# Performance work log

Hardware: AMD Instinct MI355X
Metric: run time of the kernel (lower is better)

The kernel has to match this reference:

```python
import jax, jax.numpy as jnp
import numpy as np

B, S, D, H = 4, 2048, 1024, 16
HD = D // H  # head_dim = 64


def rope(x):
    # canonical interleaved RoPE over the full feature dim, applied pre-head-split
    # x: [B, S, D]
    d = x.shape[-1]
    inv_freq = 1.0 / (10000.0 ** (jnp.arange(0, d, 2, dtype=jnp.float32) / d))  # [D/2]
    pos = jnp.arange(x.shape[1], dtype=jnp.float32)
    ang = pos[:, None] * inv_freq[None, :]          # [S, D/2]
    cos, sin = jnp.cos(ang), jnp.sin(ang)
    x1, x2 = x[..., 0::2], x[..., 1::2]             # even/odd pairs
    r1 = x1 * cos - x2 * sin
    r2 = x1 * sin + x2 * cos
    return jnp.stack([r1, r2], axis=-1).reshape(x.shape)


def setup_inputs() -> dict:
    key = jax.random.key(0)
    ks = jax.random.split(key, 9)
    s = 1.0 / np.sqrt(D)
    def lin(k):
        kw, kb = jax.random.split(k)
        W = jax.random.uniform(kw, (D, D), jnp.float32, -s, s)
        b = jax.random.uniform(kb, (D,), jnp.float32, -s, s)
        return W, b
    Wq, bq = lin(ks[0]); Wk, bk = lin(ks[1]); Wv, bv = lin(ks[2]); W0, b0 = lin(ks[3])
    x = jax.random.normal(ks[4], (B, S, D), jnp.float32)
    return {"x": x, "Wq": Wq, "bq": bq, "Wk": Wk, "bk": bk,
            "Wv": Wv, "bv": bv, "W0": W0, "b0": b0}


def reference(x, Wq, bq, Wk, bk, Wv, bv, W0, b0):
    # QKV projections (torch Linear: x @ W.T + b; here W stored as [in, out])
    q = x @ Wq + bq
    k = x @ Wk + bk
    v = x @ Wv + bv
    # RoPE applied to full d_model before head split (as in the source)
    q = rope(q)
    k = rope(k)
    # split heads -> [B, H, S, HD]
    b, s, _ = x.shape
    qh = q.reshape(b, s, H, HD).transpose(0, 2, 1, 3)
    kh = k.reshape(b, s, H, HD).transpose(0, 2, 1, 3)
    vh = v.reshape(b, s, H, HD).transpose(0, 2, 1, 3)
    scores = jnp.einsum("bhqd,bhkd->bhqk", qh, kh) / jnp.sqrt(jnp.float32(HD))
    attn = jax.nn.softmax(scores, axis=-1)  # dropout p=0.0 -> identity
    out = jnp.einsum("bhqk,bhkd->bhqd", attn, vh)
    out = out.transpose(0, 2, 1, 3).reshape(b, s, D)
    return out @ W0 + b0
```

## Files before the change

kernel.cpp:

```cpp
#include <hip/hip_runtime.h>
#include <hip/hip_bf16.h>

typedef unsigned short u16;
typedef u16 u16x8 __attribute__((ext_vector_type(8)));
typedef float f32x4 __attribute__((ext_vector_type(4)));
typedef __bf16 bf16x8 __attribute__((ext_vector_type(8)));

#define B_ 4
#define S_ 2048
#define D_ 1024
#define H_ 16
#define HD_ 64
#define M_ (B_*S_)

#if __has_builtin(__builtin_amdgcn_exp2f)
#define EXP2(x) __builtin_amdgcn_exp2f(x)
#else
#define EXP2(x) exp2f(x)
#endif

__device__ __forceinline__ f32x4 MFMA(u16x8 a, u16x8 b, f32x4 c) {
  return __builtin_amdgcn_mfma_f32_16x16x32_bf16(
      __builtin_bit_cast(bf16x8, a), __builtin_bit_cast(bf16x8, b), c, 0, 0, 0);
}

__device__ __forceinline__ u16 f2b(float f) {
  return __builtin_bit_cast(u16, __float2bfloat16(f));
}

__device__ __forceinline__ void load_lds16(const void* g, void* l) {
  __builtin_amdgcn_global_load_lds(
      (const __attribute__((address_space(1))) void*)g,
      (__attribute__((address_space(3))) void*)l, 16, 0, 0);
}

__device__ __forceinline__ unsigned int cvtpk(float lo, float hi) {
  unsigned int r;
  asm("v_cvt_pk_bf16_f32 %0, %1, %2" : "=v"(r) : "v"(lo), "v"(hi));
  return r;
}

__global__ __launch_bounds__(256) void k_rope_tab(float2* __restrict__ tab) {
  int i = blockIdx.x * 256 + threadIdx.x;
  if (i >= S_ * (D_ / 2)) return;
  int s = i >> 9;
  int f = i & 511;
  float invf = exp2f((float)f * (-13.287712379549449f / 512.0f));
  float ang = (float)s * invf;
  tab[i] = make_float2(cosf(ang), sinf(ang));
}

__global__ __launch_bounds__(256) void k_cvt(const float* __restrict__ x,
                                             u16* __restrict__ xb, int n) {
  int i = blockIdx.x * 256 + threadIdx.x;
  if (i * 4 >= n) return;
  float4 v = ((const float4*)x)[i];
  ushort4 o;
  o.x = f2b(v.x); o.y = f2b(v.y); o.z = f2b(v.z); o.w = f2b(v.w);
  ((ushort4*)xb)[i] = o;
}

__global__ __launch_bounds__(256) void k_transpose4(
    const float* __restrict__ Wq, const float* __restrict__ Wk,
    const float* __restrict__ Wv, const float* __restrict__ W0,
    u16* __restrict__ Tq, u16* __restrict__ Tk, u16* __restrict__ Tv,
    u16* __restrict__ T0) {
  const float* W = (blockIdx.z == 0) ? Wq : (blockIdx.z == 1) ? Wk
                   : (blockIdx.z == 2) ? Wv : W0;
  u16* WT = (blockIdx.z == 0) ? Tq : (blockIdx.z == 1) ? Tk
            : (blockIdx.z == 2) ? Tv : T0;
  __shared__ float t[32][33];
  int tx = threadIdx.x, ty = threadIdx.y;
  int bx = blockIdx.x * 32, by = blockIdx.y * 32;
#pragma unroll
  for (int j = 0; j < 32; j += 8)
    t[ty + j][tx] = W[(size_t)(by + ty + j) * D_ + bx + tx];
  __syncthreads();
#pragma unroll
  for (int j = 0; j < 32; j += 8)
    WT[(size_t)(bx + ty + j) * D_ + by + tx] = f2b(t[tx][ty + j]);
}

__global__ __launch_bounds__(512, 2) void k_gemm256_qkv(
    const u16* __restrict__ A, const u16* __restrict__ BT,
    const float* __restrict__ bq, const float* __restrict__ bk,
    const float* __restrict__ bv, const float2* __restrict__ tab,
    u16* __restrict__ Qh, u16* __restrict__ Kh, u16* __restrict__ Vt) {
  __shared__ __attribute__((aligned(16))) u16 Al0[16384], Al1[16384];
  __shared__ __attribute__((aligned(16))) u16 Bl0[16384], Bl1[16384];
  const int tid = threadIdx.x;
  const int lane = tid & 63, wid = tid >> 6;
  const int wm = wid >> 2, wn = wid & 3;
  const int g = lane >> 4, c = lane & 15;
  const int flat = blockIdx.x;
  const int xcd = flat & 7, idx = flat >> 3;
  const int bx = xcd * 4 + (idx & 3), by = idx >> 2;
  const int rowbase = bx * 256;

  const int rr_ = tid >> 3, slot = tid & 7;
  const int sw8 = slot ^ (rr_ & 7);
  const u16* aB = A + (size_t)(rowbase + rr_) * 1024 + sw8 * 8;
  const u16* bB = BT + (size_t)(by * 256 + rr_) * 1024 + sw8 * 8;
  const int wdst = wid * 512;

  f32x4 acc[8][4] = {};
  const int swz = (c & 7) << 3;
  const int k0o = (g * 8) ^ swz;
  const int k1o = k0o ^ 32;
  const int ArdB = (wm * 128 + c) * 64;
  const int BrdB = (wn * 64 + c) * 64;

  u16x8 bf00, bf01, bf10, bf11, bf20, bf21, bf30, bf31;

#define ISSUE_LO(NA, NB, KT)                                                 \
  load_lds16(aB + (KT), &NA[wdst]);                                          \
  load_lds16(aB + 65536 + (KT), &NA[4096 + wdst]);                           \
  load_lds16(bB + (KT), &NB[wdst]);                                          \
  load_lds16(bB + 65536 + (KT), &NB[4096 + wdst]);
#define ISSUE_HI(NA, NB, KT)                                                 \
  load_lds16(aB + 131072 + (KT), &NA[8192 + wdst]);                          \
  load_lds16(aB + 196608 + (KT), &NA[12288 + wdst]);                         \
  load_lds16(bB + 131072 + (KT), &NB[8192 + wdst]);                          \
  load_lds16(bB + 196608 + (KT), &NB[12288 + wdst]);
#define PBAR                                                                 \
  __builtin_amdgcn_sched_barrier(0);                                         \
  __builtin_amdgcn_s_barrier();                                              \
  asm volatile("s_waitcnt lgkmcnt(0)" ::: "memory");                         \
  __builtin_amdgcn_sched_barrier(0);                                         \
  __builtin_amdgcn_s_setprio(1);
#define PEND                                                                 \
  __builtin_amdgcn_s_setprio(0);                                             \
  __builtin_amdgcn_sched_barrier(0);                                         \
  __builtin_amdgcn_s_barrier();
#define LDB8(CB)                                                             \
  bf00 = *(const u16x8*)&CB[BrdB + k0o];                                     \
  bf01 = *(const u16x8*)&CB[BrdB + k1o];                                     \
  bf10 = *(const u16x8*)&CB[BrdB + 1024 + k0o];                              \
  bf11 = *(const u16x8*)&CB[BrdB + 1024 + k1o];                              \
  bf20 = *(const u16x8*)&CB[BrdB + 2048 + k0o];                              \
  bf21 = *(const u16x8*)&CB[BrdB + 2048 + k1o];                              \
  bf30 = *(const u16x8*)&CB[BrdB + 3072 + k0o];                              \
  bf31 = *(const u16x8*)&CB[BrdB + 3072 + k1o];
#define LDA4(CA, MI0)                                                        \
  a00 = *(const u16x8*)&CA[ArdB + (MI0) * 1024 + k0o];                       \
  a01 = *(const u16x8*)&CA[ArdB + (MI0) * 1024 + k1o];                       \
  a10 = *(const u16x8*)&CA[ArdB + (MI0 + 1) * 1024 + k0o];                   \
  a11 = *(const u16x8*)&CA[ArdB + (MI0 + 1) * 1024 + k1o];
#define MFMA16(MI0)                                                          \
  acc[MI0][0] = MFMA(a00, bf00, acc[MI0][0]);                                \
  acc[MI0][0] = MFMA(a01, bf01, acc[MI0][0]);                                \
  acc[MI0][1] = MFMA(a00, bf10, acc[MI0][1]);                                \
  acc[MI0][1] = MFMA(a01, bf11, acc[MI0][1]);                                \
  acc[MI0][2] = MFMA(a00, bf20, acc[MI0][2]);                                \
  acc[MI0][2] = MFMA(a01, bf21, acc[MI0][2]);                                \
  acc[MI0][3] = MFMA(a00, bf30, acc[MI0][3]);                                \
  acc[MI0][3] = MFMA(a01, bf31, acc[MI0][3]);                                \
  acc[MI0 + 1][0] = MFMA(a10, bf00, acc[MI0 + 1][0]);                        \
  acc[MI0 + 1][0] = MFMA(a11, bf01, acc[MI0 + 1][0]);                        \
  acc[MI0 + 1][1] = MFMA(a10, bf10, acc[MI0 + 1][1]);                        \
  acc[MI0 + 1][1] = MFMA(a11, bf11, acc[MI0 + 1][1]);                        \
  acc[MI0 + 1][2] = MFMA(a10, bf20, acc[MI0 + 1][2]);                        \
  acc[MI0 + 1][2] = MFMA(a11, bf21, acc[MI0 + 1][2]);                        \
  acc[MI0 + 1][3] = MFMA(a10, bf30, acc[MI0 + 1][3]);                        \
  acc[MI0 + 1][3] = MFMA(a11, bf31, acc[MI0 + 1][3]);
#define TILE(CA, CB, NA, NB, KT, STG)                                        \
  {                                                                          \
    u16x8 a00, a01, a10, a11;                                                \
    if (STG) { ISSUE_LO(NA, NB, KT) }                                        \
    LDB8(CB) LDA4(CA, 0)                                                     \
    PBAR MFMA16(0) PEND                                                      \
    if (STG) { ISSUE_HI(NA, NB, KT) }                                        \
    LDA4(CA, 2) PBAR MFMA16(2) PEND                                          \
    LDA4(CA, 4) PBAR MFMA16(4) PEND                                          \
    LDA4(CA, 6) PBAR MFMA16(6)                                               \
    __builtin_amdgcn_s_setprio(0);                                           \
    __syncthreads();                                                         \
  }

  ISSUE_LO(Al0, Bl0, 0)
  ISSUE_HI(Al0, Bl0, 0)
  __syncthreads();

#pragma unroll 1
  for (int it = 0; it < 7; ++it) {
    const int kt1 = (2 * it + 1) * 64, kt2 = (2 * it + 2) * 64;
    TILE(Al0, Bl0, Al1, Bl1, kt1, 1)
    TILE(Al1, Bl1, Al0, Bl0, kt2, 1)
  }
  TILE(Al0, Bl0, Al1, Bl1, 15 * 64, 1)
  TILE(Al1, Bl1, Al0, Bl0, 0, 0)

  const int mode = by >> 2;
  const float* bias = (mode == 0) ? bq : (mode == 1) ? bk : bv;
  u16* Cout = (mode == 0) ? Qh : (mode == 1) ? Kh : Vt;
  const int colL0 = (by & 3) * 256 + wn * 64;
  int coln[4];
  float bn[4];
#pragma unroll
  for (int ni = 0; ni < 4; ++ni) {
    coln[ni] = colL0 + ni * 16 + c;
    bn[ni] = bias[coln[ni]];
  }
  if (mode == 2) {
#pragma unroll
    for (int mi = 0; mi < 8; ++mi) {
      const int row0 = rowbase + wm * 128 + mi * 16 + g * 4;
      const int s0 = row0 & (S_ - 1);
      const int bidx = row0 >> 11;
#pragma unroll
      for (int ni = 0; ni < 4; ++ni) {
        const int h = coln[ni] >> 6, hd = coln[ni] & 63;
        ushort4 w;
        w.x = f2b(acc[mi][ni][0] + bn[ni]);
        w.y = f2b(acc[mi][ni][1] + bn[ni]);
        w.z = f2b(acc[mi][ni][2] + bn[ni]);
        w.w = f2b(acc[mi][ni][3] + bn[ni]);
        *(ushort4*)(Cout + ((size_t)(bidx * H_ + h) * HD_ + hd) * S_ + s0) = w;
      }
    }
  } else {
    const float qs = 0.18033688011112042f;
#pragma unroll
    for (int mi = 0; mi < 8; ++mi) {
#pragma unroll
      for (int rq = 0; rq < 4; ++rq) {
        const int row = rowbase + wm * 128 + mi * 16 + g * 4 + rq;
        const int s = row & (S_ - 1);
        const int bidx = row >> 11;
#pragma unroll
        for (int ni = 0; ni < 4; ++ni) {
          float v = acc[mi][ni][rq] + bn[ni];
          float2 cs = tab[(size_t)s * 512 + (coln[ni] >> 1)];
          float nb = __shfl_xor(v, 1);
          v = (lane & 1) ? (nb * cs.y + v * cs.x) : (v * cs.x - nb * cs.y);
          if (mode == 0) v *= qs;
          const int h = coln[ni] >> 6, hd = coln[ni] & 63;
          Cout[(((size_t)(bidx * H_ + h)) * S_ + s) * HD_ + hd] = f2b(v);
        }
      }
    }
  }
#undef TILE
#undef MFMA16
#undef LDA4
#undef LDB8
#undef PEND
#undef PBAR
#undef ISSUE_HI
#undef ISSUE_LO
}

__global__ __launch_bounds__(256, 2) void k_gemm_o(
    const u16* __restrict__ A, const u16* __restrict__ BT,
    const float* __restrict__ bias, float* __restrict__ Cout) {
  __shared__ __attribute__((aligned(16))) u16 Al[128 * 64];
  __shared__ __attribute__((aligned(16))) u16 Bl[128 * 64];
  const int tid = threadIdx.x;
  const int lane = tid & 63, wid = tid >> 6;
  const int wr = wid >> 1, wc = wid & 1;
  const int g = lane >> 4, c = lane & 15;
  const int flat = blockIdx.y * gridDim.x + blockIdx.x;
  const int xcd = flat & 7, idx = flat >> 3;
  const int bx = xcd * 8 + (idx & 7), by = idx >> 3;
  const int rowbase = bx * 128, colbase = by * 128;

  f32x4 acc[4][4] = {};
  const int ldr = lane >> 3;
  const int ldk = (lane & 7) * 8;

  for (int kt = 0; kt < D_; kt += 64) {
    __syncthreads();
#pragma unroll
    for (int j = 0; j < 4; ++j) {
      const int chunk = wid * 4 + j;
      const int rr = chunk * 8 + ldr;
      load_lds16(A + (size_t)(rowbase + rr) * D_ + kt + ldk, &Al[chunk * 512]);
      load_lds16(BT + (size_t)(colbase + rr) * D_ + kt + ldk, &Bl[chunk * 512]);
    }
    __syncthreads();
#pragma unroll
    for (int ks = 0; ks < 2; ++ks) {
      u16x8 a[4], b[4];
#pragma unroll
      for (int m = 0; m < 4; ++m)
        a[m] = *(const u16x8*)&Al[(wr * 64 + m * 16 + c) * 64 + ks * 32 + g * 8];
#pragma unroll
      for (int n = 0; n < 4; ++n)
        b[n] = *(const u16x8*)&Bl[(wc * 64 + n * 16 + c) * 64 + ks * 32 + g * 8];
#pragma unroll
      for (int m = 0; m < 4; ++m)
#pragma unroll
        for (int n = 0; n < 4; ++n)
          acc[m][n] = MFMA(a[m], b[n], acc[m][n]);
    }
  }

  int coln[4];
  float bn[4];
#pragma unroll
  for (int n = 0; n < 4; ++n) {
    coln[n] = colbase + wc * 64 + n * 16 + c;
    bn[n] = bias[coln[n]];
  }
#pragma unroll
  for (int m = 0; m < 4; ++m)
#pragma unroll
    for (int r = 0; r < 4; ++r) {
      const int row = rowbase + wr * 64 + m * 16 + g * 4 + r;
#pragma unroll
      for (int n = 0; n < 4; ++n)
        Cout[(size_t)row * D_ + coln[n]] = acc[m][n][r] + bn[n];
    }
}

__global__ __launch_bounds__(512, 4) void k_attn(const u16* __restrict__ Qh,
                                                 const u16* __restrict__ Kh,
                                                 const u16* __restrict__ Vt,
                                                 u16* __restrict__ AO) {
  __shared__ __attribute__((aligned(16))) u16 Kl0[4096], Kl1[4096];
  __shared__ __attribute__((aligned(16))) u16 Vl0[4096], Vl1[4096];
  __shared__ __attribute__((aligned(16))) u16 Pl[16384];
  const int tid = threadIdx.x;
  const int lane = tid & 63, wid = tid >> 6;
  const int g = lane >> 4, c = lane & 15;
  const int flat = blockIdx.x;
  const int swzid = (flat & 7) * 64 + (flat >> 3);
  const int bh = swzid >> 3, qt = swzid & 7;
  const size_t base = (size_t)bh * S_ * HD_;
  const int qr0 = qt * 256 + wid * 32;

  u16x8 qf[2][2];
#pragma unroll
  for (int qg = 0; qg < 2; ++qg)
#pragma unroll
    for (int ks = 0; ks < 2; ++ks)
      qf[qg][ks] = *(const u16x8*)(Qh + base +
                                   (size_t)(qr0 + qg * 16 + c) * HD_ +
                                   ks * 32 + g * 8);

  f32x4 o20[4] = {}, o21[4] = {};
  float L0 = 0.f, L1 = 0.f;

  const int swz = (c & 7) << 3;
  const int kb0 = c * 64 + ((g * 8) ^ swz);
  const int kb1 = c * 64 + ((32 + g * 8) ^ swz);
  const int pwA0 = wid * 2048 + ((c * 64 + 0 * 16 + g * 4) ^ swz);
  const int pwA1 = wid * 2048 + ((c * 64 + 1 * 16 + g * 4) ^ swz);
  const int pwA2 = wid * 2048 + ((c * 64 + 2 * 16 + g * 4) ^ swz);
  const int pwA3 = wid * 2048 + ((c * 64 + 3 * 16 + g * 4) ^ swz);
  const int pbA0 = wid * 2048 + kb0;
  const int pbA1 = wid * 2048 + kb1;
  const f32x4 z4 = {0.f, 0.f, 0.f, 0.f};

  const int ldrow = lane >> 3, ldslot = lane & 7;
  const int srow = wid * 8 + ldrow;
  const u16* kp0 = Kh + base + (size_t)srow * HD_ + (ldslot ^ (srow & 7)) * 8;
  const u16* vp0 = Vt + base + (size_t)srow * S_ + (ldslot ^ (srow & 7)) * 8;
  const int kdst0 = wid * 512;

#define STAGE(KP, VP)                                                        \
  {                                                                          \
    load_lds16(kp0, &KP[kdst0]); kp0 += 64 * HD_;                            \
    load_lds16(vp0, &VP[kdst0]); vp0 += 64;                                  \
  }

#define BODY(KC, VC, KP, VP)                                                 \
  {                                                                          \
    STAGE(KP, VP);                                                           \
    f32x4 s40[4], s41[4];                                                    \
    __builtin_amdgcn_s_setprio(1);                                           \
    _Pragma("unroll") for (int n = 0; n < 4; ++n) {                          \
      u16x8 kfa = *(const u16x8*)&KC[n * 1024 + kb0];                        \
      u16x8 kfb = *(const u16x8*)&KC[n * 1024 + kb1];                        \
      s40[n] = MFMA(kfa, qf[0][0], z4);                                      \
      s40[n] = MFMA(kfb, qf[0][1], s40[n]);                                  \
      s41[n] = MFMA(kfa, qf[1][0], z4);                                      \
      s41[n] = MFMA(kfb, qf[1][1], s41[n]);                                  \
    }                                                                        \
    __builtin_amdgcn_s_setprio(0);                                           \
    float rs0 = 0.f, rs1 = 0.f;                                              \
    _Pragma("unroll") for (int n = 0; n < 4; ++n) {                          \
      float p0[4], p1[4];                                                    \
      _Pragma("unroll") for (int r = 0; r < 4; ++r) {                        \
        p0[r] = EXP2(s40[n][r]); rs0 += p0[r];                               \
        p1[r] = EXP2(s41[n][r]); rs1 += p1[r];                               \
      }                                                                      \
      uint2 w0, w1;                                                          \
      w0.x = cvtpk(p0[0], p0[1]); w0.y = cvtpk(p0[2], p0[3]);                \
      w1.x = cvtpk(p1[0], p1[1]); w1.y = cvtpk(p1[2], p1[3]);                \
      const int pw = (n == 0) ? pwA0 : (n == 1) ? pwA1 : (n == 2) ? pwA2     \
                                                                  : pwA3;   \
      *(uint2*)&Pl[pw] = w0;                                                 \
      *(uint2*)&Pl[pw + 1024] = w1;                                          \
    }                                                                        \
    L0 += rs0; L1 += rs1;                                                    \
    asm volatile("s_waitcnt lgkmcnt(0)" ::: "memory");                       \
    __builtin_amdgcn_sched_barrier(0);                                       \
    __builtin_amdgcn_s_setprio(1);                                           \
    {                                                                        \
      u16x8 pa00 = *(const u16x8*)&Pl[pbA0];                                 \
      u16x8 pa01 = *(const u16x8*)&Pl[pbA1];                                 \
      u16x8 pa10 = *(const u16x8*)&Pl[pbA0 + 1024];                          \
      u16x8 pa11 = *(const u16x8*)&Pl[pbA1 + 1024];                          \
      _Pragma("unroll") for (int nd = 0; nd < 4; ++nd) {                     \
        u16x8 va0 = *(const u16x8*)&VC[nd * 1024 + kb0];                     \
        u16x8 va1 = *(const u16x8*)&VC[nd * 1024 + kb1];                     \
        o20[nd] = MFMA(va0, pa00, o20[nd]);                                  \
        o20[nd] = MFMA(va1, pa01, o20[nd]);                                  \
        o21[nd] = MFMA(va0, pa10, o21[nd]);                                  \
        o21[nd] = MFMA(va1, pa11, o21[nd]);                                  \
      }                                                                      \
    }                                                                        \
    __builtin_amdgcn_s_setprio(0);                                           \
    __syncthreads();                                                         \
  }

  STAGE(Kl0, Vl0);
  __syncthreads();

#pragma unroll 1
  for (int it = 0; it < 16; ++it) {
    BODY(Kl0, Vl0, Kl1, Vl1);
    BODY(Kl1, Vl1, Kl0, Vl0);
  }

  L0 += __shfl_xor(L0, 16);
  L0 += __shfl_xor(L0, 32);
  L1 += __shfl_xor(L1, 16);
  L1 += __shfl_xor(L1, 32);
  const float inv0 = 1.f / L0, inv1 = 1.f / L1;
  const int b = bh >> 4, h = bh & (H_ - 1);
#pragma unroll
  for (int nd = 0; nd < 4; ++nd) {
    ushort4 w;
    w.x = f2b(o20[nd][0] * inv0);
    w.y = f2b(o20[nd][1] * inv0);
    w.z = f2b(o20[nd][2] * inv0);
    w.w = f2b(o20[nd][3] * inv0);
    *(ushort4*)(AO + ((size_t)(b * S_ + qr0 + c)) * D_ + h * HD_ + nd * 16 +
                g * 4) = w;
    ushort4 w2;
    w2.x = f2b(o21[nd][0] * inv1);
    w2.y = f2b(o21[nd][1] * inv1);
    w2.z = f2b(o21[nd][2] * inv1);
    w2.w = f2b(o21[nd][3] * inv1);
    *(ushort4*)(AO + ((size_t)(b * S_ + qr0 + 16 + c)) * D_ + h * HD_ +
                nd * 16 + g * 4) = w2;
  }
#undef BODY
#undef STAGE
}

extern "C" void kernel_launch(void* const* d_in, const int* in_sizes, int n_in,
                              void* d_out, int out_size, void* d_ws,
                              size_t ws_size, hipStream_t stream) {
  const float* x  = (const float*)d_in[0];
  const float* Wq = (const float*)d_in[1];
  const float* bq = (const float*)d_in[2];
  const float* Wk = (const float*)d_in[3];
  const float* bk = (const float*)d_in[4];
  const float* Wv = (const float*)d_in[5];
  const float* bv = (const float*)d_in[6];
  const float* W0 = (const float*)d_in[7];
  const float* b0 = (const float*)d_in[8];
  float* out = (float*)d_out;

  char* ws = (char*)d_ws;
  const size_t MiB = (size_t)1 << 20;
  float2* tab = (float2*)(ws + 0);
  u16* xb  = (u16*)(ws + 8 * MiB);
  u16* WqT = (u16*)(ws + 24 * MiB);
  u16* WkT = (u16*)(ws + 26 * MiB);
  u16* WvT = (u16*)(ws + 28 * MiB);
  u16* W0T = (u16*)(ws + 30 * MiB);
  u16* Qh  = (u16*)(ws + 32 * MiB);
  u16* Kh  = (u16*)(ws + 48 * MiB);
  u16* Vt  = (u16*)(ws + 64 * MiB);
  u16* AO  = (u16*)(ws + 80 * MiB);

  k_rope_tab<<<4096, 256, 0, stream>>>(tab);
  k_cvt<<<(M_ * D_ / 4 + 255) / 256, 256, 0, stream>>>(x, xb, M_ * D_);
  k_transpose4<<<dim3(32, 32, 4), dim3(32, 8), 0, stream>>>(
      Wq, Wk, Wv, W0, WqT, WkT, WvT, W0T);
  k_gemm256_qkv<<<384, 512, 0, stream>>>(xb, WqT, bq, bk, bv, tab, Qh, Kh, Vt);
  k_attn<<<512, 512, 0, stream>>>(Qh, Kh, Vt, AO);
  k_gemm_o<<<dim3(64, 8), 256, 0, stream>>>(AO, W0T, b0, out);
}
```

Baseline: 191.5 us.

## Merge prep kernels into one launch and single-buffer the QKV GEMM LDS

Combines the RoPE table, input bf16 conversion and weight transpose kernels into a single k_prep launch that dispatches on block index, saving two kernel launches. The QKV GEMM drops its LDS double buffer: each k-step now issues all global-to-LDS loads, waits at a barrier, then computes. This halves LDS use, which may allow more resident blocks, but it removes the overlap of the next tile's loads with the current MFMA work, so load latency is exposed on every k iteration.

```diff
diff --git a/kernel.cpp b/kernel.cpp
--- a/kernel.cpp
+++ b/kernel.cpp
@@ -40,45 +40,43 @@
   return r;
 }
 
-__global__ __launch_bounds__(256) void k_rope_tab(float2* __restrict__ tab) {
-  int i = blockIdx.x * 256 + threadIdx.x;
-  if (i >= S_ * (D_ / 2)) return;
-  int s = i >> 9;
-  int f = i & 511;
-  float invf = exp2f((float)f * (-13.287712379549449f / 512.0f));
-  float ang = (float)s * invf;
-  tab[i] = make_float2(cosf(ang), sinf(ang));
-}
-
-__global__ __launch_bounds__(256) void k_cvt(const float* __restrict__ x,
-                                             u16* __restrict__ xb, int n) {
-  int i = blockIdx.x * 256 + threadIdx.x;
-  if (i * 4 >= n) return;
-  float4 v = ((const float4*)x)[i];
-  ushort4 o;
-  o.x = f2b(v.x); o.y = f2b(v.y); o.z = f2b(v.z); o.w = f2b(v.w);
-  ((ushort4*)xb)[i] = o;
-}
-
-__global__ __launch_bounds__(256) void k_transpose4(
+__global__ __launch_bounds__(256) void k_prep(
+    const float* __restrict__ x, u16* __restrict__ xb,
     const float* __restrict__ Wq, const float* __restrict__ Wk,
     const float* __restrict__ Wv, const float* __restrict__ W0,
     u16* __restrict__ Tq, u16* __restrict__ Tk, u16* __restrict__ Tv,
-    u16* __restrict__ T0) {
-  const float* W = (blockIdx.z == 0) ? Wq : (blockIdx.z == 1) ? Wk
-                   : (blockIdx.z == 2) ? Wv : W0;
-  u16* WT = (blockIdx.z == 0) ? Tq : (blockIdx.z == 1) ? Tk
-            : (blockIdx.z == 2) ? Tv : T0;
+    u16* __restrict__ T0, float2* __restrict__ tab) {
   __shared__ float t[32][33];
-  int tx = threadIdx.x, ty = threadIdx.y;
-  int bx = blockIdx.x * 32, by = blockIdx.y * 32;
-#pragma unroll
-  for (int j = 0; j < 32; j += 8)
-    t[ty + j][tx] = W[(size_t)(by + ty + j) * D_ + bx + tx];
-  __syncthreads();
-#pragma unroll
-  for (int j = 0; j < 32; j += 8)
-    WT[(size_t)(bx + ty + j) * D_ + by + tx] = f2b(t[tx][ty + j]);
+  const int bid = blockIdx.x;
+  const int tid = threadIdx.x;
+  if (bid < 4096) {
+    int i = bid * 256 + tid;
+    int s = i >> 9;
+    int f = i & 511;
+    float invf = exp2f((float)f * (-13.287712379549449f / 512.0f));
+    float ang = (float)s * invf;
+    tab[i] = make_float2(cosf(ang), sinf(ang));
+  } else if (bid < 12288) {
+    int i = (bid - 4096) * 256 + tid;
+    float4 v = ((const float4*)x)[i];
+    ushort4 o;
+    o.x = f2b(v.x); o.y = f2b(v.y); o.z = f2b(v.z); o.w = f2b(v.w);
+    ((ushort4*)xb)[i] = o;
+  } else {
+    const int bid2 = bid - 12288;
+    const int z = bid2 >> 10, rem = bid2 & 1023;
+    const float* W = (z == 0) ? Wq : (z == 1) ? Wk : (z == 2) ? Wv : W0;
+    u16* WT = (z == 0) ? Tq : (z == 1) ? Tk : (z == 2) ? Tv : T0;
+    const int tx = tid & 31, ty = tid >> 5;
+    const int bx = (rem & 31) * 32, by = (rem >> 5) * 32;
+#pragma unroll
+    for (int j = 0; j < 32; j += 8)
+      t[ty + j][tx] = W[(size_t)(by + ty + j) * D_ + bx + tx];
+    __syncthreads();
+#pragma unroll
+    for (int j = 0; j < 32; j += 8)
+      WT[(size_t)(bx + ty + j) * D_ + by + tx] = f2b(t[tx][ty + j]);
+  }
 }
 
 __global__ __launch_bounds__(512, 2) void k_gemm256_qkv(
@@ -86,8 +84,8 @@
     const float* __restrict__ bq, const float* __restrict__ bk,
     const float* __restrict__ bv, const float2* __restrict__ tab,
     u16* __restrict__ Qh, u16* __restrict__ Kh, u16* __restrict__ Vt) {
-  __shared__ __attribute__((aligned(16))) u16 Al0[16384], Al1[16384];
-  __shared__ __attribute__((aligned(16))) u16 Bl0[16384], Bl1[16384];
+  __shared__ __attribute__((aligned(16))) u16 Al[16384];
+  __shared__ __attribute__((aligned(16))) u16 Bl[16384];
   const int tid = threadIdx.x;
   const int lane = tid & 63, wid = tid >> 6;
   const int wm = wid >> 2, wn = wid & 3;
@@ -112,16 +110,15 @@
 
   u16x8 bf00, bf01, bf10, bf11, bf20, bf21, bf30, bf31;
 
-#define ISSUE_LO(NA, NB, KT)                                                 \
-  load_lds16(aB + (KT), &NA[wdst]);                                          \
-  load_lds16(aB + 65536 + (KT), &NA[4096 + wdst]);                           \
-  load_lds16(bB + (KT), &NB[wdst]);                                          \
-  load_lds16(bB + 65536 + (KT), &NB[4096 + wdst]);
-#define ISSUE_HI(NA, NB, KT)                                                 \
-  load_lds16(aB + 131072 + (KT), &NA[8192 + wdst]);                          \
-  load_lds16(aB + 196608 + (KT), &NA[12288 + wdst]);                         \
-  load_lds16(bB + 131072 + (KT), &NB[8192 + wdst]);                          \
-  load_lds16(bB + 196608 + (KT), &NB[12288 + wdst]);
+#define ISSUE_ALL(KT)                                                        \
+  load_lds16(aB + (KT), &Al[wdst]);                                          \
+  load_lds16(aB + 65536 + (KT), &Al[4096 + wdst]);                           \
+  load_lds16(aB + 131072 + (KT), &Al[8192 + wdst]);                          \
+  load_lds16(aB + 196608 + (KT), &Al[12288 + wdst]);                         \
+  load_lds16(bB + (KT), &Bl[wdst]);                                          \
+  load_lds16(bB + 65536 + (KT), &Bl[4096 + wdst]);                           \
+  load_lds16(bB + 131072 + (KT), &Bl[8192 + wdst]);                          \
+  load_lds16(bB + 196608 + (KT), &Bl[12288 + wdst]);
 #define PBAR                                                                 \
   __builtin_amdgcn_sched_barrier(0);                                         \
   __builtin_amdgcn_s_barrier();                                              \
@@ -132,20 +129,20 @@
   __builtin_amdgcn_s_setprio(0);                                             \
   __builtin_amdgcn_sched_barrier(0);                                         \
   __builtin_amdgcn_s_barrier();
-#define LDB8(CB)                                                             \
-  bf00 = *(const u16x8*)&CB[BrdB + k0o];                                     \
-  bf01 = *(const u16x8*)&CB[BrdB + k1o];                                     \
-  bf10 = *(const u16x8*)&CB[BrdB + 1024 + k0o];                              \
-  bf11 = *(const u16x8*)&CB[BrdB + 1024 + k1o];                              \
-  bf20 = *(const u16x8*)&CB[BrdB + 2048 + k0o];                              \
-  bf21 = *(const u16x8*)&CB[BrdB + 2048 + k1o];                              \
-  bf30 = *(const u16x8*)&CB[BrdB + 3072 + k0o];                              \
-  bf31 = *(const u16x8*)&CB[BrdB + 3072 + k1o];
-#define LDA4(CA, MI0)                                                        \
-  a00 = *(const u16x8*)&CA[ArdB + (MI0) * 1024 + k0o];                       \
-  a01 = *(const u16x8*)&CA[ArdB + (MI0) * 1024 + k1o];                       \
-  a10 = *(const u16x8*)&CA[ArdB + (MI0 + 1) * 1024 + k0o];                   \
-  a11 = *(const u16x8*)&CA[ArdB + (MI0 + 1) * 1024 + k1o];
+#define LDB8                                                                 \
+  bf00 = *(const u16x8*)&Bl[BrdB + k0o];                                     \
+  bf01 = *(const u16x8*)&Bl[BrdB + k1o];                                     \
+  bf10 = *(const u16x8*)&Bl[BrdB + 1024 + k0o];                              \
+  bf11 = *(const u16x8*)&Bl[BrdB + 1024 + k1o];                              \
+  bf20 = *(const u16x8*)&Bl[BrdB + 2048 + k0o];                              \
+  bf21 = *(const u16x8*)&Bl[BrdB + 2048 + k1o];                              \
+  bf30 = *(const u16x8*)&Bl[BrdB + 3072 + k0o];                              \
+  bf31 = *(const u16x8*)&Bl[BrdB + 3072 + k1o];
+#define LDA4(MI0)                                                            \
+  a00 = *(const u16x8*)&Al[ArdB + (MI0) * 1024 + k0o];                       \
+  a01 = *(const u16x8*)&Al[ArdB + (MI0) * 1024 + k1o];                       \
+  a10 = *(const u16x8*)&Al[ArdB + (MI0 + 1) * 1024 + k0o];                   \
+  a11 = *(const u16x8*)&Al[ArdB + (MI0 + 1) * 1024 + k1o];
 #define MFMA16(MI0)                                                          \
   acc[MI0][0] = MFMA(a00, bf00, acc[MI0][0]);                                \
   acc[MI0][0] = MFMA(a01, bf01, acc[MI0][0]);                                \
@@ -163,32 +160,20 @@
   acc[MI0 + 1][2] = MFMA(a11, bf21, acc[MI0 + 1][2]);                        \
   acc[MI0 + 1][3] = MFMA(a10, bf30, acc[MI0 + 1][3]);                        \
   acc[MI0 + 1][3] = MFMA(a11, bf31, acc[MI0 + 1][3]);
-#define TILE(CA, CB, NA, NB, KT, STG)                                        \
-  {                                                                          \
-    u16x8 a00, a01, a10, a11;                                                \
-    if (STG) { ISSUE_LO(NA, NB, KT) }                                        \
-    LDB8(CB) LDA4(CA, 0)                                                     \
-    PBAR MFMA16(0) PEND                                                      \
-    if (STG) { ISSUE_HI(NA, NB, KT) }                                        \
-    LDA4(CA, 2) PBAR MFMA16(2) PEND                                          \
-    LDA4(CA, 4) PBAR MFMA16(4) PEND                                          \
-    LDA4(CA, 6) PBAR MFMA16(6)                                               \
-    __builtin_amdgcn_s_setprio(0);                                           \
-    __syncthreads();                                                         \
-  }
-
-  ISSUE_LO(Al0, Bl0, 0)
-  ISSUE_HI(Al0, Bl0, 0)
-  __syncthreads();
 
 #pragma unroll 1
-  for (int it = 0; it < 7; ++it) {
-    const int kt1 = (2 * it + 1) * 64, kt2 = (2 * it + 2) * 64;
-    TILE(Al0, Bl0, Al1, Bl1, kt1, 1)
-    TILE(Al1, Bl1, Al0, Bl0, kt2, 1)
-  }
-  TILE(Al0, Bl0, Al1, Bl1, 15 * 64, 1)
-  TILE(Al1, Bl1, Al0, Bl0, 0, 0)
+  for (int kt = 0; kt < 16; ++kt) {
+    if (kt) __syncthreads();
+    ISSUE_ALL(kt * 64)
+    __syncthreads();
+    u16x8 a00, a01, a10, a11;
+    LDB8 LDA4(0)
+    PBAR MFMA16(0) PEND
+    LDA4(2) PBAR MFMA16(2) PEND
+    LDA4(4) PBAR MFMA16(4) PEND
+    LDA4(6) PBAR MFMA16(6)
+    __builtin_amdgcn_s_setprio(0);
+  }
 
   const int mode = by >> 2;
   const float* bias = (mode == 0) ? bq : (mode == 1) ? bk : bv;
@@ -240,14 +225,12 @@
       }
     }
   }
-#undef TILE
 #undef MFMA16
 #undef LDA4
 #undef LDB8
 #undef PEND
 #undef PBAR
-#undef ISSUE_HI
-#undef ISSUE_LO
+#undef ISSUE_ALL
 }
 
 __global__ __launch_bounds__(256, 2) void k_gemm_o(
@@ -478,10 +461,8 @@
   u16* Vt  = (u16*)(ws + 64 * MiB);
   u16* AO  = (u16*)(ws + 80 * MiB);
 
-  k_rope_tab<<<4096, 256, 0, stream>>>(tab);
-  k_cvt<<<(M_ * D_ / 4 + 255) / 256, 256, 0, stream>>>(x, xb, M_ * D_);
-  k_transpose4<<<dim3(32, 32, 4), dim3(32, 8), 0, stream>>>(
-      Wq, Wk, Wv, W0, WqT, WkT, WvT, W0T);
+  k_prep<<<16384, 256, 0, stream>>>(x, xb, Wq, Wk, Wv, W0,
+                                    WqT, WkT, WvT, W0T, tab);
   k_gemm256_qkv<<<384, 512, 0, stream>>>(xb, WqT, bq, bk, bv, tab, Qh, Kh, Vt);
   k_attn<<<512, 512, 0, stream>>>(Qh, Kh, Vt, AO);
   k_gemm_o<<<dim3(64, 8), 256, 0, stream>>>(AO, W0T, b0, out);
```

Result: slower. 204.4 us (+6.8%).
